# Kernel optimization log

Hardware: AMD Instinct MI355X
Metric: run time of the kernel (lower is better)

The kernel has to match this reference:

```python
import jax, jax.numpy as jnp
import numpy as np
import math

N_WIRES = 8
DIM = 2 ** N_WIRES  # 256

# Pauli-Z sign table: wire 0 is the most-significant axis of the statevector.
_idx = np.arange(DIM)
_SIGNS = np.stack([1.0 - 2.0 * ((_idx >> (N_WIRES - 1 - w)) & 1) for w in range(N_WIRES)], axis=1).astype(np.float32)  # [256, 8]


def _cnot(state, c, t):
    # state: [N, 2, 2, ..., 2]; flip target axis where control bit == 1
    s0, s1 = jnp.split(state, 2, axis=1 + c)
    s1 = jnp.flip(s1, axis=1 + t)
    return jnp.concatenate([s0, s1], axis=1 + c)


def _quantum_heads(x, theta):
    """Simulate the QLayer circuit. x: [N, 8] -> PauliZ expectations [N, 8].

    Circuit: RX(x_i) then RX(theta_i) on wire i (commute -> RX(x_i+theta_i)),
    CNOT chain (0,1)...(6,7),(7,0), MeasureAll(PauliZ).
    """
    phi = 0.5 * (x + theta)  # RX half-angle
    c = jnp.cos(phi)
    s = jnp.sin(phi)
    # RX(a)|0> = cos(a/2)|0> - i sin(a/2)|1>
    amps = jax.lax.complex(jnp.stack([c, jnp.zeros_like(c)], axis=-1),
                           jnp.stack([jnp.zeros_like(s), -s], axis=-1))  # [N, 8, 2] complex64
    # Product state as rank-8 tensor [N, 2, ..., 2]
    state = amps[:, 0]
    for w in range(1, N_WIRES):
        state = state[..., None] * amps[:, w].reshape((-1,) + (1,) * w + (2,))
    # Entangling CNOT ring
    for w in range(N_WIRES - 1):
        state = _cnot(state, w, w + 1)
    state = _cnot(state, N_WIRES - 1, 0)
    probs = jnp.abs(state.reshape(-1, DIM)) ** 2  # [N, 256]
    return probs @ jnp.asarray(_SIGNS)  # [N, 8]


def setup_inputs() -> dict:
    key = jax.random.key(0)
    k1, k2, k3, k4 = jax.random.split(key, 4)
    B, S, E = 32, 512, 64
    return {
        "x": jax.random.normal(k1, (B, S, E), dtype=jnp.float32),
        "theta": jax.random.normal(k2, (N_WIRES,), dtype=jnp.float32),
        "W": jax.random.normal(k3, (E, E), dtype=jnp.float32) * 0.05,
        "b": jax.random.normal(k4, (E,), dtype=jnp.float32) * 0.05,
    }


def reference(x, theta, W, b):
    B, S, E = x.shape
    H = E // N_WIRES  # num_heads
    # q = k = v: same deterministic quantum projection applied to the same x.
    z = _quantum_heads(x.reshape(B * S * H, N_WIRES), theta).reshape(B, S, H, N_WIRES)
    scale = 1.0 / math.sqrt(E // H)
    # NOTE: matmul over last dims -> attention across heads within each token.
    scores = jnp.einsum('bshd,bstd->bsht', z, z) * scale  # [B, S, H, H]
    attn = jax.nn.softmax(scores, axis=-1)
    out = jnp.einsum('bsht,bstd->bshd', attn, z).reshape(B, S, E)
    return out @ W.T + b
```

## Files before the change

kernel.cpp:

```cpp
#include <hip/hip_runtime.h>


#define BLK_TOK 64

typedef __attribute__((ext_vector_type(8))) short short8;
typedef __attribute__((ext_vector_type(4))) float f32x4;

__device__ inline unsigned short f2bf(float f) {
    unsigned u = __float_as_uint(f);
    u += 0x7FFF + ((u >> 16) & 1);
    return (unsigned short)(u >> 16);
}

__device__ inline short8 pack_bf16x8(float4 a, float4 b) {
    short8 r;
    r[0] = (short)f2bf(a.x); r[1] = (short)f2bf(a.y);
    r[2] = (short)f2bf(a.z); r[3] = (short)f2bf(a.w);
    r[4] = (short)f2bf(b.x); r[5] = (short)f2bf(b.y);
    r[6] = (short)f2bf(b.z); r[7] = (short)f2bf(b.w);
    return r;
}

__global__ __launch_bounds__(1024)
void mhaq_fused9(const float* __restrict__ x,
                 const float* __restrict__ theta,
                 const float* __restrict__ W,
                 const float* __restrict__ bias,
                 float* __restrict__ out,
                 int n_tokens)
{
    __shared__ __align__(16) float          zs[BLK_TOK * 68];
    __shared__ __align__(16) unsigned short os[BLK_TOK * 72];

    const int tid = threadIdx.x;
    const int tl  = tid >> 4;
    const int s   = tid & 15;
    const int h   = s >> 1;
    const int q   = s & 1;
    const int blockbase = blockIdx.x * BLK_TOK;
    const int token = blockbase + tl;

    const int wave = tid >> 6;
    const int lane = tid & 63;
    const int lr   = lane & 15;
    const int lg   = lane >> 4;
    const int tile = wave >> 2;
    const int jq   = wave & 3;
    const int j    = jq * 16 + lr;

    const float tw0 = theta[0], tw1 = theta[1], tw2 = theta[2], tw3 = theta[3];
    const float tw4 = theta[4], tw5 = theta[5], tw6 = theta[6], tw7 = theta[7];
    const float tq0 = q ? tw4 : tw0;
    const float tq1 = q ? tw5 : tw1;
    const float tq2 = q ? tw6 : tw2;
    const float tq3 = q ? tw7 : tw3;

    float4 xv = make_float4(0.f, 0.f, 0.f, 0.f);
    if (token < n_tokens)
        xv = *reinterpret_cast<const float4*>(x + (size_t)token * 64 + s * 4);

    const float bj = bias[j];
    short8 bfrag0, bfrag1;
    {
        const float4* __restrict__ Wv = reinterpret_cast<const float4*>(W);
        const int base = j * 16 + lg * 2;
        float4 w00 = Wv[base],     w01 = Wv[base + 1];
        float4 w10 = Wv[base + 8], w11 = Wv[base + 9];
        bfrag0 = pack_bf16x8(w00, w01);
        bfrag1 = pack_bf16x8(w10, w11);
    }

    float cq0 = __cosf(xv.x + tq0);
    float cq1 = __cosf(xv.y + tq1);
    float cq2 = __cosf(xv.z + tq2);
    float cq3 = __cosf(xv.w + tq3);
    float cp0 = __shfl_xor(cq0, 1, 64);
    float cp1 = __shfl_xor(cq1, 1, 64);
    float cp2 = __shfl_xor(cq2, 1, 64);
    float cp3 = __shfl_xor(cq3, 1, 64);
    float l0 = q ? cp0 : cq0;
    float l1 = q ? cp1 : cq1;
    float l2 = q ? cp2 : cq2;
    float l3 = q ? cp3 : cq3;
    float h0 = q ? cq0 : cp0;
    float h1 = q ? cq1 : cp1;
    float h2 = q ? cq2 : cp2;
    float h3 = q ? cq3 : cp3;
    float p1 = l0 * l1;
    float p2 = p1 * l2;
    float p3 = p2 * l3;
    float p4 = p3 * h0;
    float p5 = p4 * h1;
    float p6 = p5 * h2;
    float p7 = p6 * h3;
    float t12  = l1 * l2;
    float t123 = t12 * l3;
    float hh   = h0 * h1;
    float hh2  = hh * h2;
    float hh3  = hh2 * h3;
    float s1   = t123 * hh3;
    float4 zst = q ? make_float4(p4, p5, p6, p7)
                   : make_float4(s1, p1, p2, p3);
    *reinterpret_cast<float4*>(zs + tl * 68 + s * 4) = zst;
    __syncthreads();

    {
        const float* zrow = zs + tl * 68;
        const float zh[8] = {s1, p1, p2, p3, p4, p5, p6, p7};

        float zt8[32];
        #pragma unroll
        for (int i = 0; i < 8; ++i)
            *reinterpret_cast<float4*>(&zt8[i * 4]) =
                *reinterpret_cast<const float4*>(&zrow[q * 32 + i * 4]);

        float zo[16];
        #pragma unroll
        for (int tt = 0; tt < 4; ++tt)
            *reinterpret_cast<float4*>(&zo[tt * 4]) =
                *reinterpret_cast<const float4*>(
                    &zrow[((1 - q) * 4 + tt) * 8 + q * 4]);

        const float scale = 0.35355339059327373f;
        float e[4];
        float psum = 0.f;
        #pragma unroll
        for (int tt = 0; tt < 4; ++tt) {
            float sd = 0.f;
            #pragma unroll
            for (int d = 0; d < 8; ++d)
                sd = fmaf(zh[d], zt8[tt * 8 + d], sd);
            e[tt] = __expf(sd * scale);
            psum += e[tt];
        }
        float tot = psum + __shfl_xor(psum, 1, 64);
        float inv = 1.0f / tot;

        float ep[4];
        #pragma unroll
        for (int tt = 0; tt < 4; ++tt)
            ep[tt] = __shfl_xor(e[tt], 1, 64);

        unsigned short oh[4];
        #pragma unroll
        for (int dd = 0; dd < 4; ++dd) {
            float acc = 0.f;
            #pragma unroll
            for (int tt = 0; tt < 4; ++tt) {
                float zown = q ? zt8[tt * 8 + 4 + dd] : zt8[tt * 8 + dd];
                acc = fmaf(e[tt],  zown,            acc);
                acc = fmaf(ep[tt], zo[tt * 4 + dd], acc);
            }
            oh[dd] = f2bf(acc * inv);
        }
        *reinterpret_cast<ushort4*>(&os[tl * 72 + h * 8 + q * 4]) =
            make_ushort4(oh[0], oh[1], oh[2], oh[3]);
    }
    __syncthreads();

    {
        const unsigned short* orow = &os[(tile * 16 + lr) * 72];
        short8 afrag0 = *reinterpret_cast<const short8*>(&orow[lg * 8]);
        short8 afrag1 = *reinterpret_cast<const short8*>(&orow[32 + lg * 8]);
        f32x4 acc = {bj, bj, bj, bj};
        acc = __builtin_amdgcn_mfma_f32_16x16x32_bf16(afrag0, bfrag0, acc, 0, 0, 0);
        acc = __builtin_amdgcn_mfma_f32_16x16x32_bf16(afrag1, bfrag1, acc, 0, 0, 0);
        #pragma unroll
        for (int r = 0; r < 4; ++r) {
            int trow = blockbase + tile * 16 + lg * 4 + r;
            if (trow < n_tokens)
                out[(size_t)trow * 64 + j] = acc[r];
        }
    }
}

extern "C" void kernel_launch(void* const* d_in, const int* in_sizes, int n_in,
                              void* d_out, int out_size, void* d_ws, size_t ws_size,
                              hipStream_t stream)
{
    const float* x     = (const float*)d_in[0];
    const float* theta = (const float*)d_in[1];
    const float* W     = (const float*)d_in[2];
    const float* b     = (const float*)d_in[3];
    float* out         = (float*)d_out;

    const int n_tokens = in_sizes[0] / 64;
    const int blocks   = (n_tokens + BLK_TOK - 1) / BLK_TOK;
    mhaq_fused9<<<blocks, 1024, 0, stream>>>(x, theta, W, b, out, n_tokens);
}
```

Baseline: 10.56 us.

## Shrink blocks to 16 tokens and replace first block barrier with wave-local wait

The launch shape changes from 1024-thread blocks covering 64 tokens to 256-thread blocks covering 16 tokens, with one MFMA tile per block and launch bounds allowing 4 blocks per CU. The first __syncthreads is replaced by an LDS waitcnt plus a scheduling barrier. This is valid because each token's 16 threads sit inside one wave and read only their own token's row. The x load is issued first, and the W bf16 packing is deferred until just before the MFMA to shorten the dependency chain at kernel start. In exchange, every block re-reads the full W and bias, which is four times the redundant traffic, though it should hit in L2.

```diff
diff --git a/kernel.cpp b/kernel.cpp
--- a/kernel.cpp
+++ b/kernel.cpp
@@ -1,7 +1,7 @@
 #include <hip/hip_runtime.h>
 
 
-#define BLK_TOK 64
+#define TOK_PER_BLK 16
 
 typedef __attribute__((ext_vector_type(8))) short short8;
 typedef __attribute__((ext_vector_type(4))) float f32x4;
@@ -21,32 +21,34 @@
     return r;
 }
 
-__global__ __launch_bounds__(1024)
-void mhaq_fused9(const float* __restrict__ x,
-                 const float* __restrict__ theta,
-                 const float* __restrict__ W,
-                 const float* __restrict__ bias,
-                 float* __restrict__ out,
-                 int n_tokens)
+__global__ __launch_bounds__(256, 4)
+void mhaq_fused11(const float* __restrict__ x,
+                  const float* __restrict__ theta,
+                  const float* __restrict__ W,
+                  const float* __restrict__ bias,
+                  float* __restrict__ out,
+                  int n_tokens)
 {
-    __shared__ __align__(16) float          zs[BLK_TOK * 68];
-    __shared__ __align__(16) unsigned short os[BLK_TOK * 72];
+    __shared__ __align__(16) float          zs[TOK_PER_BLK * 68];
+    __shared__ __align__(16) unsigned short os[TOK_PER_BLK * 72];
 
     const int tid = threadIdx.x;
     const int tl  = tid >> 4;
     const int s   = tid & 15;
     const int h   = s >> 1;
     const int q   = s & 1;
-    const int blockbase = blockIdx.x * BLK_TOK;
+    const int blockbase = blockIdx.x * TOK_PER_BLK;
     const int token = blockbase + tl;
 
+    const int lane = tid & 63;
     const int wave = tid >> 6;
-    const int lane = tid & 63;
     const int lr   = lane & 15;
     const int lg   = lane >> 4;
-    const int tile = wave >> 2;
-    const int jq   = wave & 3;
-    const int j    = jq * 16 + lr;
+    const int j    = wave * 16 + lr;
+
+    float4 xv = make_float4(0.f, 0.f, 0.f, 0.f);
+    if (token < n_tokens)
+        xv = *reinterpret_cast<const float4*>(x + (size_t)token * 64 + s * 4);
 
     const float tw0 = theta[0], tw1 = theta[1], tw2 = theta[2], tw3 = theta[3];
     const float tw4 = theta[4], tw5 = theta[5], tw6 = theta[6], tw7 = theta[7];
@@ -55,19 +57,14 @@
     const float tq2 = q ? tw6 : tw2;
     const float tq3 = q ? tw7 : tw3;
 
-    float4 xv = make_float4(0.f, 0.f, 0.f, 0.f);
-    if (token < n_tokens)
-        xv = *reinterpret_cast<const float4*>(x + (size_t)token * 64 + s * 4);
-
-    const float bj = bias[j];
-    short8 bfrag0, bfrag1;
+    float4 wf00, wf01, wf10, wf11;
+    float  bj;
     {
         const float4* __restrict__ Wv = reinterpret_cast<const float4*>(W);
         const int base = j * 16 + lg * 2;
-        float4 w00 = Wv[base],     w01 = Wv[base + 1];
-        float4 w10 = Wv[base + 8], w11 = Wv[base + 9];
-        bfrag0 = pack_bf16x8(w00, w01);
-        bfrag1 = pack_bf16x8(w10, w11);
+        wf00 = Wv[base];     wf01 = Wv[base + 1];
+        wf10 = Wv[base + 8]; wf11 = Wv[base + 9];
+        bj = bias[j];
     }
 
     float cq0 = __cosf(xv.x + tq0);
@@ -102,7 +99,9 @@
     float4 zst = q ? make_float4(p4, p5, p6, p7)
                    : make_float4(s1, p1, p2, p3);
     *reinterpret_cast<float4*>(zs + tl * 68 + s * 4) = zst;
-    __syncthreads();
+
+    asm volatile("s_waitcnt lgkmcnt(0)" ::: "memory");
+    __builtin_amdgcn_sched_barrier(0);
 
     {
         const float* zrow = zs + tl * 68;
@@ -159,7 +158,9 @@
     __syncthreads();
 
     {
-        const unsigned short* orow = &os[(tile * 16 + lr) * 72];
+        short8 bfrag0 = pack_bf16x8(wf00, wf01);
+        short8 bfrag1 = pack_bf16x8(wf10, wf11);
+        const unsigned short* orow = &os[lr * 72];
         short8 afrag0 = *reinterpret_cast<const short8*>(&orow[lg * 8]);
         short8 afrag1 = *reinterpret_cast<const short8*>(&orow[32 + lg * 8]);
         f32x4 acc = {bj, bj, bj, bj};
@@ -167,7 +168,7 @@
         acc = __builtin_amdgcn_mfma_f32_16x16x32_bf16(afrag1, bfrag1, acc, 0, 0, 0);
         #pragma unroll
         for (int r = 0; r < 4; ++r) {
-            int trow = blockbase + tile * 16 + lg * 4 + r;
+            int trow = blockbase + lg * 4 + r;
             if (trow < n_tokens)
                 out[(size_t)trow * 64 + j] = acc[r];
         }
@@ -185,6 +186,6 @@
     float* out         = (float*)d_out;
 
     const int n_tokens = in_sizes[0] / 64;
-    const int blocks   = (n_tokens + BLK_TOK - 1) / BLK_TOK;
-    mhaq_fused9<<<blocks, 1024, 0, stream>>>(x, theta, W, b, out, n_tokens);
+    const int blocks   = (n_tokens + TOK_PER_BLK - 1) / TOK_PER_BLK;
+    mhaq_fused11<<<blocks, 256, 0, stream>>>(x, theta, W, b, out, n_tokens);
 }
```

New measurement: 9.797 us. -7.2%, faster.
